# Performance work log

Hardware: AMD Instinct MI355X
Metric: run time of the kernel (lower is better)

## Reference

```python
import jax, jax.numpy as jnp
import numpy as np

EPS = 1e-6


def _mp_match(reps, att, kernel):
    """BiMPM multi-perspective match.
    reps: (B,L,D); att: (B,L,D) or (B,1,D); kernel: (M,D).
    Returns (B,L,1+M): [tanh(sum(reps*att)), tanh(sum_d reps*kernel_m*att)].
    """
    prod = reps * att                                   # (B,L,D)
    cos = jnp.tanh(jnp.sum(prod, axis=-1, keepdims=True))   # (B,L,1)
    mp = jnp.tanh(jnp.einsum('bld,md->blm', prod, kernel))  # (B,L,M)
    return jnp.concatenate([cos, mp], axis=-1)


def setup_inputs() -> dict:
    key = jax.random.key(0)
    ks = jax.random.split(key, 12)
    B, Llt, Lrt, D, M, A = 32, 128, 128, 512, 64, 128
    H = D // 2
    u = lambda k, shape: jax.random.uniform(k, shape, jnp.float32, -0.05, 0.05)  # keras 'uniform' init
    return {
        'reps_lt': jax.random.normal(ks[0], (B, Llt, D), jnp.float32),
        'h_lt_fw': jax.random.normal(ks[1], (B, H), jnp.float32),
        'h_lt_bw': jax.random.normal(ks[2], (B, H), jnp.float32),
        'reps_rt': jax.random.normal(ks[3], (B, Lrt, D), jnp.float32),
        'h_rt_fw': jax.random.normal(ks[4], (B, H), jnp.float32),
        'h_rt_bw': jax.random.normal(ks[5], (B, H), jnp.float32),
        'kernel_full': u(ks[6], (M, D)),
        'kernel_mpool': u(ks[7], (M, D)),
        'attn_w1': u(ks[8], (D, A)),
        'diag_w': u(ks[9], (A,)),
        'kernel_att': u(ks[10], (M, D)),
        'kernel_maxatt': u(ks[11], (M, D)),
    }


def reference(reps_lt, h_lt_fw, h_lt_bw, reps_rt, h_rt_fw, h_rt_bw,
              kernel_full, kernel_mpool, attn_w1, diag_w,
              kernel_att, kernel_maxatt):
    # ---- full match: each left timestep vs last BiLSTM state of right ----
    h_rt = jnp.concatenate([h_rt_fw, h_rt_bw], axis=-1)[:, None, :]  # (B,1,D)
    full = _mp_match(reps_lt, h_rt, kernel_full)                     # (B,Ll,1+M)

    # ---- max-pooling match ----
    # t[b,r,l,m] = tanh(sum_d R[b,r,d]*K[m,d]*L[b,l,d]); max over right positions r
    r_scaled = jnp.einsum('brd,md->brmd', reps_rt, kernel_mpool)     # (B,Lr,M,D)
    t = jnp.tanh(jnp.einsum('brmd,bld->brlm', r_scaled, reps_lt))    # (B,Lr,Ll,M)
    mpool = jnp.max(t, axis=1)                                       # (B,Ll,M)

    # ---- attentive match ----
    a_lt = jnp.tanh(reps_lt @ attn_w1) * diag_w                      # (B,Ll,A)
    a_rt = jnp.tanh(reps_rt @ attn_w1)                               # (B,Lr,A)
    scores = jnp.einsum('bla,bra->blr', a_lt, a_rt)                  # (B,Ll,Lr)
    probs = jax.nn.softmax(scores, axis=-1)
    att = jnp.einsum('blr,brd->bld', probs, reps_rt)                 # (B,Ll,D)
    attentive = _mp_match(reps_lt, att, kernel_att)                  # (B,Ll,1+M)

    # ---- max-attentive match ----
    num = jnp.einsum('bld,brd->blr', reps_lt, reps_rt)
    n_lt = jnp.sqrt(jnp.maximum(jnp.sum(reps_lt * reps_lt, -1), EPS))[:, :, None]
    n_rt = jnp.sqrt(jnp.maximum(jnp.sum(reps_rt * reps_rt, -1), EPS))[:, None, :]
    rel = num / n_rt / n_lt                                          # (B,Ll,Lr)
    idx = jnp.argmax(rel, axis=2)                                    # (B,Ll) int
    max_att = jnp.take_along_axis(reps_rt, idx[:, :, None], axis=1)  # (B,Ll,D)
    maxatt = _mp_match(reps_lt, max_att, kernel_maxatt)              # (B,Ll,1+M)

    return jnp.concatenate([full, mpool, attentive, maxatt], axis=-1)  # (B,Ll,3+4M)
```

## Files before the change

### kernel.cpp

```cpp
#include <hip/hip_runtime.h>
#include <hip/hip_bf16.h>
#include <math.h>
#include <stdint.h>

typedef __attribute__((ext_vector_type(8))) short short8;
typedef __attribute__((ext_vector_type(4))) float float4v;

#define DEV static __device__ __forceinline__

DEV float bflo(unsigned int u) { union { unsigned int i; float f; } v; v.i = u << 16; return v.f; }
DEV float bfhi(unsigned int u) { union { unsigned int i; float f; } v; v.i = u & 0xffff0000u; return v.f; }
DEV unsigned short f2bf(float f) {
    union { float f; unsigned int i; } v; v.f = f;
    unsigned int x = v.i;
    return (unsigned short)((x + 0x7fffu + ((x >> 16) & 1u)) >> 16);
}
DEV unsigned int pack2(float a, float b) { return (unsigned int)f2bf(a) | ((unsigned int)f2bf(b) << 16); }
#if __has_builtin(__builtin_amdgcn_cvt_pk_bf16_f32)
DEV unsigned int pack2_fast(float a, float b) {
    typedef __attribute__((ext_vector_type(2))) short short2v;
    short2v r = __builtin_amdgcn_cvt_pk_bf16_f32(a, b);
    union { short2v s; unsigned int u; } v; v.s = r; return v.u;
}
#else
DEV unsigned int pack2_fast(float a, float b) { return pack2(a, b); }
#endif
DEV void unpack8(uint4 u, float* f) {
    f[0]=bflo(u.x); f[1]=bfhi(u.x); f[2]=bflo(u.y); f[3]=bfhi(u.y);
    f[4]=bflo(u.z); f[5]=bfhi(u.z); f[6]=bflo(u.w); f[7]=bfhi(u.w);
}

DEV void async16(const unsigned short* g, unsigned short* l) {
    __builtin_amdgcn_global_load_lds(
        (const __attribute__((address_space(1))) unsigned int*)g,
        (__attribute__((address_space(3))) unsigned int*)l, 16, 0, 0);
}

__global__ __launch_bounds__(256) void prep_kernel(const float* __restrict__ lt,
                                                   const float* __restrict__ rt,
                                                   const float* __restrict__ kf,
                                                   const float* __restrict__ kmp,
                                                   const float* __restrict__ ka,
                                                   const float* __restrict__ km,
                                                   const float* __restrict__ w1,
                                                   unsigned short* __restrict__ ltb,
                                                   unsigned short* __restrict__ rtb,
                                                   unsigned short* __restrict__ kb,
                                                   unsigned short* __restrict__ w1t,
                                                   double* __restrict__ rsq) {
    __shared__ double ws2[2][2];
    __shared__ float tile[32][33];
    int bid = blockIdx.x, t = threadIdx.x;
    if (bid < 1024) {
        bool isRt = bid >= 512;
        int base = (isRt ? (bid - 512) : bid) * 8;
        int rl = t >> 7;
        int c  = t & 127;
        const float* srcb = isRt ? rt : lt;
        unsigned short* dstb = isRt ? rtb : ltb;
        #pragma unroll
        for (int p = 0; p < 4; ++p) {
            int row = base + p * 2 + rl;
            const float* src = srcb + (size_t)row * 512;
            float4 v = *(const float4*)(src + c * 4);
            ushort4 o;
            o.x = f2bf(v.x); o.y = f2bf(v.y); o.z = f2bf(v.z); o.w = f2bf(v.w);
            *(ushort4*)(dstb + (size_t)row * 512 + c * 4) = o;
            if (isRt) {
                double s = (double)v.x * v.x + (double)v.y * v.y
                         + (double)v.z * v.z + (double)v.w * v.w;
                #pragma unroll
                for (int off = 1; off < 64; off <<= 1) s += __shfl_xor(s, off, 64);
                if ((c & 63) == 0) ws2[rl][c >> 6] = s;
                __syncthreads();
                if (c == 0) rsq[row] = 1.0 / sqrt(ws2[rl][0] + ws2[rl][1]);
                __syncthreads();
            }
        }
    } else if (bid < 1152) {
        int kbk = bid - 1024;
        int ksel = kbk >> 5;
        const float* src = (ksel == 0) ? kf : (ksel == 1) ? kmp : (ksel == 2) ? ka : km;
        int off = (kbk & 31) * 1024 + t * 4;
        float4 v = *(const float4*)(src + off);
        ushort4 o;
        o.x = f2bf(v.x); o.y = f2bf(v.y); o.z = f2bf(v.z); o.w = f2bf(v.w);
        *(ushort4*)(kb + ksel * 32768 + off) = o;
    } else {
        int b2 = bid - 1152;
        int d0 = (b2 & 15) * 32, a0 = (b2 >> 4) * 32;
        int r = t >> 5, c = t & 31;
        #pragma unroll
        for (int i = 0; i < 32; i += 8)
            tile[r + i][c] = w1[(size_t)(d0 + r + i) * 128 + a0 + c];
        __syncthreads();
        #pragma unroll
        for (int i = 0; i < 32; i += 8)
            w1t[(size_t)(a0 + r + i) * 512 + d0 + c] = f2bf(tile[c][r + i]);
    }
}

__global__ __launch_bounds__(256, 3) void uber_kernel(
        const unsigned short* __restrict__ ltb,
        const unsigned short* __restrict__ rtb,
        const unsigned short* __restrict__ kmb,
        const unsigned short* __restrict__ w1t,
        const float* __restrict__ diag,
        unsigned short* __restrict__ a_all,
        const float* __restrict__ ltf,
        const float* __restrict__ rtf,
        const double* __restrict__ rsq,
        int* __restrict__ idxout,
        float* __restrict__ out) {
    __shared__ __align__(16) unsigned char smem[52224];
    int bx = blockIdx.x;
    int t = threadIdx.x;
    int wave = t >> 6, lane = t & 63;
    int q = lane >> 4, col = lane & 15, kq = q * 8;

    if (bx < 2048) {
        int xcd = bx & 7, jj = bx >> 3;
        int b = xcd * 4 + (jj >> 6);
        int m = jj & 63;
        unsigned short* ltS = (unsigned short*)smem;
        unsigned short* rtL = (unsigned short*)(smem + 16384);
        float (*mx)[2] = (float(*)[2])(smem + 16384 + 32768);
        int wl = wave & 1, wr = wave >> 1;
        const unsigned short* ltp = ltb + (size_t)b * 65536;
        const unsigned short* rtp = rtb + (size_t)b * 65536;
        const unsigned short* kr = kmb + (size_t)m * 512;
        int srow = t >> 3, cg8 = t & 7, cg = cg8 * 8;
        int gsw = (cg8 ^ (srow & 7)) * 8;
        int wbase = (t & ~63) * 8;

        #pragma unroll
        for (int it = 0; it < 4; ++it)
            async16(rtp + (size_t)(it * 32 + srow) * 512 + gsw,
                    rtL + it * 2048 + wbase);
        uint4 pk = *(const uint4*)(kr + cg);
        uint4 plt[4];
        #pragma unroll
        for (int it = 0; it < 4; ++it)
            plt[it] = *(const uint4*)(ltp + (size_t)(it * 32 + srow) * 512 + cg);

        float4v acc[4][4] = {};
        for (int k0i = 0; k0i < 8; ++k0i) {
            float kf8[8]; unpack8(pk, kf8);
            #pragma unroll
            for (int it = 0; it < 4; ++it) {
                int row = it * 32 + srow;
                float lf[8]; unpack8(plt[it], lf);
                uint4 s;
                s.x = pack2_fast(lf[0] * kf8[0], lf[1] * kf8[1]);
                s.y = pack2_fast(lf[2] * kf8[2], lf[3] * kf8[3]);
                s.z = pack2_fast(lf[4] * kf8[4], lf[5] * kf8[5]);
                s.w = pack2_fast(lf[6] * kf8[6], lf[7] * kf8[7]);
                *(uint4*)&ltS[row * 64 + gsw] = s;
            }
            __syncthreads();
            if (k0i < 7) {
                int k0n = (k0i + 1) * 64;
                int bofs = ((k0i + 1) & 1) * 8192;
                #pragma unroll
                for (int it = 0; it < 4; ++it)
                    async16(rtp + (size_t)(it * 32 + srow) * 512 + k0n + gsw,
                            rtL + bofs + it * 2048 + wbase);
                pk = *(const uint4*)(kr + k0n + cg);
                #pragma unroll
                for (int it = 0; it < 4; ++it)
                    plt[it] = *(const uint4*)(ltp + (size_t)(it * 32 + srow) * 512 + k0n + cg);
            }
            const unsigned short* rb = rtL + (k0i & 1) * 8192;
            #pragma unroll
            for (int kk = 0; kk < 64; kk += 32) {
                short8 af[4], bfr[4];
                #pragma unroll
                for (int i = 0; i < 4; ++i) {
                    int rowA = wl * 64 + i * 16 + col;
                    int slotA = ((kk >> 3) + q) ^ (rowA & 7);
                    af[i] = *(const short8*)&ltS[rowA * 64 + slotA * 8];
                }
                #pragma unroll
                for (int j = 0; j < 4; ++j) {
                    int row = wr * 64 + j * 16 + col;
                    int slot = ((kk >> 3) + q) ^ (row & 7);
                    bfr[j] = *(const short8*)&rb[row * 64 + slot * 8];
                }
                #pragma unroll
                for (int i = 0; i < 4; ++i)
                    #pragma unroll
                    for (int j = 0; j < 4; ++j)
                        acc[i][j] = __builtin_amdgcn_mfma_f32_16x16x32_bf16(af[i], bfr[j], acc[i][j], 0, 0, 0);
            }
            __syncthreads();
        }
        #pragma unroll
        for (int i = 0; i < 4; ++i)
            #pragma unroll
            for (int ii = 0; ii < 4; ++ii) {
                float v = fmaxf(fmaxf(acc[i][0][ii], acc[i][1][ii]), fmaxf(acc[i][2][ii], acc[i][3][ii]));
                #pragma unroll
                for (int off = 1; off < 16; off <<= 1) v = fmaxf(v, __shfl_xor(v, off, 64));
                if (col == 0) mx[wl * 64 + i * 16 + q * 4 + ii][wr] = v;
            }
        __syncthreads();
        if (t < 128)
            out[((size_t)(b * 128 + t)) * 259 + 65 + m] = tanhf(fmaxf(mx[t][0], mx[t][1]));

    } else if (bx < 2560) {
        int idA = bx - 2048;
        int xcd = idA & 7, jj = idA >> 3;
        int b = xcd * 4 + (jj >> 4);
        int L0 = (jj & 15) * 8;
        float* ltS = (float*)smem;
        float* buf = (float*)(smem + 16384);
        double* dvs = (double*)(smem + 49152);
        float* wv1 = (float*)(smem + 49152 + 128);
        float* wv2 = wv1 + 16;
        int* wi1 = (int*)(wv2 + 16);
        int* wi2 = wi1 + 16;
        int* candi = wi2 + 16;
        {
            int row = t >> 5, c0 = (t & 31) * 16;
            const float* src = ltf + ((size_t)(b * 128 + L0 + row)) * 512 + c0;
            #pragma unroll
            for (int i = 0; i < 4; ++i)
                *(float4*)&ltS[row * 512 + c0 + i * 4] = *(const float4*)(src + i * 4);
        }
        int lg = t >> 7;
        int rg = (t >> 2) & 31;
        int ds = t & 3;
        float acc[4][4] = {{0.f}};
        for (int p = 0; p < 8; ++p) {
            __syncthreads();
            {
                int row = t >> 1, c0 = (t & 1) * 32;
                const float* src = rtf + ((size_t)(b * 128 + row)) * 512 + p * 64 + c0;
                float f[32];
                #pragma unroll
                for (int i = 0; i < 8; ++i)
                    *(float4*)&f[i * 4] = *(const float4*)(src + i * 4);
                int base = row * 64;
                #pragma unroll
                for (int gg = 0; gg < 4; ++gg) {
                    int g = (t & 1) * 4 + gg;
                    int o = ((g ^ (row & 7)) * 8);
                    #pragma unroll
                    for (int k = 0; k < 8; ++k) buf[base + o + k] = f[gg * 8 + k];
                }
            }
            __syncthreads();
            #pragma unroll
            for (int sub = 0; sub < 2; ++sub) {
                int dloc = ds * 16 + sub * 8;
                int dglob = p * 64 + dloc;
                float a[4][8];
                #pragma unroll
                for (int i = 0; i < 4; ++i)
                    #pragma unroll
                    for (int k = 0; k < 8; ++k) a[i][k] = ltS[(lg * 4 + i) * 512 + dglob + k];
                int g = dloc >> 3;
                #pragma unroll
                for (int j = 0; j < 4; ++j) {
                    int r = rg + j * 32;
                    const float* rp = &buf[r * 64 + ((g ^ (r & 7)) * 8)];
                    float rv[8];
                    #pragma unroll
                    for (int k = 0; k < 8; ++k) rv[k] = rp[k];
                    #pragma unroll
                    for (int i = 0; i < 4; ++i)
                        #pragma unroll
                        for (int k = 0; k < 8; ++k)
                            acc[i][j] = fmaf(a[i][k], rv[k], acc[i][j]);
                }
            }
        }
        #pragma unroll
        for (int i = 0; i < 4; ++i)
            #pragma unroll
            for (int j = 0; j < 4; ++j) {
                acc[i][j] += __shfl_xor(acc[i][j], 1, 64);
                acc[i][j] += __shfl_xor(acc[i][j], 2, 64);
            }
        float v1[4], v2[4]; int i1[4], i2[4];
        #pragma unroll
        for (int i = 0; i < 4; ++i) {
            v1[i] = -3.0e38f; v2[i] = -3.0e38f; i1[i] = 0; i2[i] = 1;
            #pragma unroll
            for (int j = 0; j < 4; ++j) {
                int r = rg + j * 32;
                float s = acc[i][j] * (float)rsq[b * 128 + r];
                if (s > v1[i]) { v2[i] = v1[i]; i2[i] = i1[i]; v1[i] = s; i1[i] = r; }
                else if (s > v2[i]) { v2[i] = s; i2[i] = r; }
            }
        }
        #pragma unroll
        for (int off = 4; off < 64; off <<= 1) {
            #pragma unroll
            for (int i = 0; i < 4; ++i) {
                float u1 = __shfl_xor(v1[i], off, 64); int j1 = __shfl_xor(i1[i], off, 64);
                float u2 = __shfl_xor(v2[i], off, 64); int j2 = __shfl_xor(i2[i], off, 64);
                if (u1 > v1[i]) {
                    float ov = v1[i]; int oi = i1[i];
                    v1[i] = u1; i1[i] = j1;
                    if (u2 > ov) { v2[i] = u2; i2[i] = j2; } else { v2[i] = ov; i2[i] = oi; }
                } else if (u1 > v2[i]) { v2[i] = u1; i2[i] = j1; }
            }
        }
        if (lane == 0) {
            #pragma unroll
            for (int i = 0; i < 4; ++i) {
                int l = lg * 4 + i, h = wave & 1;
                wv1[l * 2 + h] = v1[i]; wi1[l * 2 + h] = i1[i];
                wv2[l * 2 + h] = v2[i]; wi2[l * 2 + h] = i2[i];
            }
        }
        __syncthreads();
        if (t < 8) {
            float a1 = wv1[t * 2], a2 = wv2[t * 2]; int ai1 = wi1[t * 2], ai2 = wi2[t * 2];
            float b1 = wv1[t * 2 + 1], b2 = wv2[t * 2 + 1]; int bi1 = wi1[t * 2 + 1], bi2 = wi2[t * 2 + 1];
            int ri1, ri2;
            if (b1 > a1) {
                ri1 = bi1;
                if (b2 > a1) { ri2 = bi2; } else { ri2 = ai1; }
            } else {
                ri1 = ai1;
                if (b1 > a2) { ri2 = bi1; } else { ri2 = ai2; }
            }
            candi[t * 2] = ri1; candi[t * 2 + 1] = ri2;
            (void)a2; (void)b2; (void)ai2; (void)bi2;
        }
        __syncthreads();
        {
            int dotid = t >> 4;
            int sub = t & 15;
            int l = dotid >> 1, c = dotid & 1;
            int r = candi[l * 2 + c];
            const float* lrow = ltf + ((size_t)(b * 128 + L0 + l)) * 512;
            const float* rrow = rtf + ((size_t)(b * 128 + r)) * 512;
            double s = 0.0;
            #pragma unroll 8
            for (int k = 0; k < 32; ++k) {
                int d = sub * 32 + k;
                s = fma((double)lrow[d], (double)rrow[d], s);
            }
            #pragma unroll
            for (int off = 1; off < 16; off <<= 1) s += __shfl_xor(s, off, 64);
            if (sub == 0) dvs[l * 2 + c] = s * rsq[b * 128 + r];
        }
        __syncthreads();
        if (t < 8) {
            int ia = candi[t * 2], ib = candi[t * 2 + 1];
            double va = dvs[t * 2], vb = dvs[t * 2 + 1];
            int res = (vb > va || (vb == va && ib < ia)) ? ib : ia;
            idxout[b * 128 + L0 + t] = res;
        }

    } else {
        int R0 = (bx - 2560) * 32;
        unsigned short (*aS)[72] = (unsigned short(*)[72])smem;
        unsigned short (*bS)[72] = (unsigned short(*)[72])(smem + 4608);
        float* diagS = (float*)(smem + 4608 + 18432);
        int wl = wave & 1, wr = wave >> 1;
        if (t < 128) diagS[t] = diag[t];
        const unsigned short* src = (R0 < 4096) ? (ltb + (size_t)R0 * 512) : (rtb + (size_t)(R0 - 4096) * 512);
        float4v acc[4] = {};
        for (int k0 = 0; k0 < 512; k0 += 64) {
            {
                int row = t >> 3, cg = (t & 7) * 8;
                *(uint4*)&aS[row][cg] = *(const uint4*)(src + (size_t)row * 512 + k0 + cg);
            }
            #pragma unroll
            for (int it = 0; it < 4; ++it) {
                int id = it * 256 + t;
                int row = id >> 3, cg = (id & 7) * 8;
                *(uint4*)&bS[row][cg] = *(const uint4*)(w1t + (size_t)row * 512 + k0 + cg);
            }
            __syncthreads();
            #pragma unroll
            for (int kk = 0; kk < 64; kk += 32) {
                short8 af = *(const short8*)&aS[wl * 16 + col][kk + kq];
                #pragma unroll
                for (int j = 0; j < 4; ++j) {
                    short8 bf = *(const short8*)&bS[wr * 64 + j * 16 + col][kk + kq];
                    acc[j] = __builtin_amdgcn_mfma_f32_16x16x32_bf16(af, bf, acc[j], 0, 0, 0);
                }
            }
            __syncthreads();
        }
        bool isLt = (R0 < 4096);
        #pragma unroll
        for (int j = 0; j < 4; ++j)
            #pragma unroll
            for (int ii = 0; ii < 4; ++ii) {
                int rowl = wl * 16 + q * 4 + ii;
                int n = wr * 64 + j * 16 + col;
                float v = tanhf(acc[j][ii]);
                if (isLt) v *= diagS[n];
                a_all[((size_t)(R0 + rowl)) * 128 + n] = f2bf(v);
            }
    }
}

__global__ __launch_bounds__(512, 4) void tail_kernel(
        const unsigned short* __restrict__ a_all,
        const unsigned short* __restrict__ rtb,
        const float* __restrict__ ltf,
        const unsigned short* __restrict__ kb,
        const float* __restrict__ hfw,
        const float* __restrict__ hbw,
        const int* __restrict__ idxp,
        float* __restrict__ out) {
    __shared__ __align__(16) unsigned char smem[81664];
    int bx = blockIdx.x;
    int t = threadIdx.x;
    int wave = t >> 6, lane = t & 63;
    int q = lane >> 4, col = lane & 15, kq = q * 8;

    if (bx < 256) {
        int b = bx & 31, lg = bx >> 5;
        int L0 = lg * 16;
        unsigned short (*altS)[136]  = (unsigned short(*)[136])(smem);
        unsigned short (*artS)[136]  = (unsigned short(*)[136])(smem + 4352);
        unsigned short (*rtS)[512]   = (unsigned short(*)[512])(smem + 39168);
        unsigned short (*prodsF)[520]= (unsigned short(*)[520])(smem + 55552);
        float (*P)[132]  = (float(*)[132])(smem + 72192);
        float (*pmax)[8] = (float(*)[8])(smem + 80640);
        float (*psum)[8] = (float(*)[8])(smem + 81152);
        const unsigned short* kb_att = kb + 2 * 32768;

        if (t < 256) {
            int row = t >> 4, c0 = (t & 15) * 8;
            *(uint4*)&altS[row][c0] = *(const uint4*)(a_all + ((size_t)(b * 128 + L0 + row)) * 128 + c0);
        }
        {
            int row = t >> 2, c0 = (t & 3) * 32;
            const unsigned short* src = a_all + ((size_t)(4096 + b * 128 + row)) * 128 + c0;
            #pragma unroll
            for (int i = 0; i < 4; ++i)
                *(uint4*)&artS[row][c0 + i * 8] = *(const uint4*)(src + i * 8);
        }
        __syncthreads();

        float4v acc = {};
        #pragma unroll
        for (int kk = 0; kk < 128; kk += 32) {
            short8 af = *(const short8*)&altS[col][kk + kq];
            short8 bf = *(const short8*)&artS[wave * 16 + col][kk + kq];
            acc = __builtin_amdgcn_mfma_f32_16x16x32_bf16(af, bf, acc, 0, 0, 0);
        }
        float m4[4], p4[4];
        #pragma unroll
        for (int ii = 0; ii < 4; ++ii) {
            float v = acc[ii];
            #pragma unroll
            for (int off = 1; off < 16; off <<= 1) v = fmaxf(v, __shfl_xor(v, off, 64));
            m4[ii] = v;
        }
        if (col == 0) {
            #pragma unroll
            for (int ii = 0; ii < 4; ++ii) pmax[q * 4 + ii][wave] = m4[ii];
        }
        __syncthreads();
        #pragma unroll
        for (int ii = 0; ii < 4; ++ii) {
            float M = pmax[q * 4 + ii][0];
            #pragma unroll
            for (int w = 1; w < 8; ++w) M = fmaxf(M, pmax[q * 4 + ii][w]);
            p4[ii] = expf(acc[ii] - M);
            float s = p4[ii];
            #pragma unroll
            for (int off = 1; off < 16; off <<= 1) s += __shfl_xor(s, off, 64);
            m4[ii] = s;
        }
        if (col == 0) {
            #pragma unroll
            for (int ii = 0; ii < 4; ++ii) psum[q * 4 + ii][wave] = m4[ii];
        }
        __syncthreads();
        #pragma unroll
        for (int ii = 0; ii < 4; ++ii) {
            float S = psum[q * 4 + ii][0] + psum[q * 4 + ii][1] + psum[q * 4 + ii][2] + psum[q * 4 + ii][3]
                    + psum[q * 4 + ii][4] + psum[q * 4 + ii][5] + psum[q * 4 + ii][6] + psum[q * 4 + ii][7];
            P[q * 4 + ii][wave * 16 + col] = p4[ii] / S;
        }

        int l = t >> 5, cd = t & 31;
        float a8[2][8] = {{0.f}};
        for (int rcb = 0; rcb < 128; rcb += 16) {
            __syncthreads();
            {
                int row = t >> 5, c0 = (t & 31) * 16;
                const unsigned short* src = rtb + ((size_t)(b * 128 + rcb + row)) * 512 + c0;
                *(uint4*)&rtS[row][c0] = *(const uint4*)src;
                *(uint4*)&rtS[row][c0 + 8] = *(const uint4*)(src + 8);
            }
            __syncthreads();
            for (int rr = 0; rr < 16; ++rr) {
                float pr = P[l][rcb + rr];
                #pragma unroll
                for (int pass = 0; pass < 2; ++pass) {
                    uint4 u = *(const uint4*)&rtS[rr][pass * 256 + cd * 8];
                    float f[8]; unpack8(u, f);
                    #pragma unroll
                    for (int k = 0; k < 8; ++k) a8[pass][k] += pr * f[k];
                }
            }
        }

        int grow = b * 128 + L0 + l;
        const float* ltrow = ltf + (size_t)grow * 512;
        float csum = 0.f;
        #pragma unroll
        for (int pass = 0; pass < 2; ++pass) {
            int d0 = pass * 256 + cd * 8;
            float lf[8];
            *(float4*)&lf[0] = *(const float4*)(ltrow + d0);
            *(float4*)&lf[4] = *(const float4*)(ltrow + d0 + 4);
            float pf[8];
            #pragma unroll
            for (int k = 0; k < 8; ++k) { pf[k] = lf[k] * a8[pass][k]; csum += pf[k]; }
            uint4 o;
            o.x = pack2(pf[0], pf[1]); o.y = pack2(pf[2], pf[3]);
            o.z = pack2(pf[4], pf[5]); o.w = pack2(pf[6], pf[7]);
            *(uint4*)&prodsF[l][d0] = o;
        }
        #pragma unroll
        for (int off = 1; off < 32; off <<= 1) csum += __shfl_xor(csum, off, 64);
        if (cd == 0) out[(size_t)grow * 259 + 129] = tanhf(csum);

        unsigned short* Ks = &artS[0][0];
        float* red = (float*)&rtS[0][0];
        for (int half = 0; half < 2; ++half) {
            __syncthreads();
            {
                int row = t >> 4, c0 = (t & 15) * 32;
                const unsigned short* src = kb_att + ((size_t)(half * 32 + row)) * 512 + c0;
                #pragma unroll
                for (int i = 0; i < 4; ++i)
                    *(uint4*)&Ks[row * 520 + c0 + i * 8] = *(const uint4*)(src + i * 8);
            }
            __syncthreads();
            float4v pacc[2] = {};
            #pragma unroll
            for (int kk = 0; kk < 64; kk += 32) {
                short8 af = *(const short8*)&prodsF[col][wave * 64 + kk + kq];
                #pragma unroll
                for (int j = 0; j < 2; ++j) {
                    short8 bf = *(const short8*)&Ks[(j * 16 + col) * 520 + wave * 64 + kk + kq];
                    pacc[j] = __builtin_amdgcn_mfma_f32_16x16x32_bf16(af, bf, pacc[j], 0, 0, 0);
                }
            }
            #pragma unroll
            for (int j = 0; j < 2; ++j)
                #pragma unroll
                for (int ii = 0; ii < 4; ++ii)
                    red[((wave * 2 + j) * 16 + q * 4 + ii) * 16 + col] = pacc[j][ii];
            __syncthreads();
            {
                int ll = t >> 5, jm = t & 31;
                int j = jm >> 4, mc = jm & 15;
                float s = 0.f;
                #pragma unroll
                for (int w = 0; w < 8; ++w) s += red[((w * 2 + j) * 16 + ll) * 16 + mc];
                out[((size_t)(b * 128 + L0 + ll)) * 259 + 130 + half * 32 + jm] = tanhf(s);
            }
        }

    } else {
        int idB = bx - 256;
        int lg = idB & 7, b = (idB >> 3) & 31;
        int mode = (idB >> 8) ? 2 : 0;
        int L0 = lg * 16;
        unsigned short (*prods)[520] = (unsigned short(*)[520])smem;
        unsigned short* Ks = (unsigned short*)(smem + 16640);
        float* red = (float*)(smem + 49920);
        const unsigned short* Kp = kb + (size_t)((mode == 0) ? 0 : 3 * 32768);
        int obase = (mode == 0) ? 0 : 194;

        if (t < 256) {
            int l = t >> 4, c = t & 15;
            int grow = b * 128 + L0 + l;
            const float* ltrow = ltf + (size_t)grow * 512;
            const unsigned short* avrow = 0;
            if (mode == 2) avrow = rtb + ((size_t)(b * 128 + idxp[grow])) * 512;
            float csum = 0.f;
            #pragma unroll
            for (int pass = 0; pass < 4; ++pass) {
                int d0 = pass * 128 + c * 8;
                float lf[8], af[8], pf[8];
                *(float4*)&lf[0] = *(const float4*)(ltrow + d0);
                *(float4*)&lf[4] = *(const float4*)(ltrow + d0 + 4);
                if (mode == 0) {
                    const float* h = (d0 < 256) ? (hfw + b * 256 + d0) : (hbw + b * 256 + d0 - 256);
                    *(float4*)&af[0] = *(const float4*)h;
                    *(float4*)&af[4] = *(const float4*)(h + 4);
                } else {
                    uint4 av = *(const uint4*)(avrow + d0);
                    unpack8(av, af);
                }
                #pragma unroll
                for (int k = 0; k < 8; ++k) { pf[k] = lf[k] * af[k]; csum += pf[k]; }
                uint4 o;
                o.x = pack2(pf[0], pf[1]); o.y = pack2(pf[2], pf[3]);
                o.z = pack2(pf[4], pf[5]); o.w = pack2(pf[6], pf[7]);
                *(uint4*)&prods[l][d0] = o;
            }
            #pragma unroll
            for (int off = 1; off < 16; off <<= 1) csum += __shfl_xor(csum, off, 64);
            if (c == 0) out[(size_t)grow * 259 + obase] = tanhf(csum);
        }
        for (int half = 0; half < 2; ++half) {
            {
                int row = t >> 4, c0 = (t & 15) * 32;
                const unsigned short* src = Kp + ((size_t)(half * 32 + row)) * 512 + c0;
                #pragma unroll
                for (int i = 0; i < 4; ++i)
                    *(uint4*)&Ks[row * 520 + c0 + i * 8] = *(const uint4*)(src + i * 8);
            }
            __syncthreads();
            float4v acc2[2] = {};
            #pragma unroll
            for (int kk = 0; kk < 64; kk += 32) {
                short8 af = *(const short8*)&prods[col][wave * 64 + kk + kq];
                #pragma unroll
                for (int j = 0; j < 2; ++j) {
                    short8 bf = *(const short8*)&Ks[(j * 16 + col) * 520 + wave * 64 + kk + kq];
                    acc2[j] = __builtin_amdgcn_mfma_f32_16x16x32_bf16(af, bf, acc2[j], 0, 0, 0);
                }
            }
            #pragma unroll
            for (int j = 0; j < 2; ++j)
                #pragma unroll
                for (int ii = 0; ii < 4; ++ii)
                    red[((wave * 2 + j) * 16 + q * 4 + ii) * 16 + col] = acc2[j][ii];
            __syncthreads();
            {
                int ll = t >> 5, jm = t & 31;
                int j = jm >> 4, mc = jm & 15;
                float s = 0.f;
                #pragma unroll
                for (int w = 0; w < 8; ++w) s += red[((w * 2 + j) * 16 + ll) * 16 + mc];
                out[((size_t)(b * 128 + L0 + ll)) * 259 + obase + 1 + half * 32 + jm] = tanhf(s);
            }
            __syncthreads();
        }
    }
}

extern "C" void kernel_launch(void* const* d_in, const int* in_sizes, int n_in,
                              void* d_out, int out_size, void* d_ws, size_t ws_size,
                              hipStream_t stream) {
    const float* lt  = (const float*)d_in[0];
    const float* rt  = (const float*)d_in[3];
    const float* hfw = (const float*)d_in[4];
    const float* hbw = (const float*)d_in[5];
    const float* kf  = (const float*)d_in[6];
    const float* kmp = (const float*)d_in[7];
    const float* w1  = (const float*)d_in[8];
    const float* dia = (const float*)d_in[9];
    const float* ka  = (const float*)d_in[10];
    const float* km  = (const float*)d_in[11];
    float* out = (float*)d_out;

    char* wsb = (char*)d_ws;
    unsigned short* ltb16 = (unsigned short*)(wsb);
    unsigned short* rtb16 = (unsigned short*)(wsb + 4194304);
    unsigned short* kb16  = (unsigned short*)(wsb + 8388608);
    unsigned short* w1t   = (unsigned short*)(wsb + 8650752);
    unsigned short* a_all = (unsigned short*)(wsb + 8781824);
    double*         rsq   = (double*)(wsb + 15073280);
    int*            idx   = (int*)(wsb + 15106048);

    prep_kernel<<<1216, 256, 0, stream>>>(lt, rt, kf, kmp, ka, km, w1, ltb16, rtb16, kb16, w1t, rsq);
    uber_kernel<<<2816, 256, 0, stream>>>(ltb16, rtb16, kb16 + 32768, w1t, dia, a_all,
                                          lt, rt, rsq, idx, out);
    tail_kernel<<<768, 512, 0, stream>>>(a_all, rtb16, lt, kb16, hfw, hbw, idx, out);
}
```

Measured before the change: 188.1 us.

## Compute attentive weighted sum with bf16 MFMA using transposed right reps

Replaces the scalar FMA loop that builds the attention-weighted right representation in the tail kernel with bf16 MFMA tiles. Probabilities are stored as bf16 in shared memory. The prep kernel gains a transpose of reps_rt into a d-major bf16 buffer that is loaded asynchronously with an XOR swizzle. This trades an extra prep pass and bf16 rounding of probabilities for much less ALU work in the tail.

```diff
diff --git a/kernel.cpp b/kernel.cpp
--- a/kernel.cpp
+++ b/kernel.cpp
@@ -47,6 +47,7 @@
                                                    unsigned short* __restrict__ rtb,
                                                    unsigned short* __restrict__ kb,
                                                    unsigned short* __restrict__ w1t,
+                                                   unsigned short* __restrict__ rtbT,
                                                    double* __restrict__ rsq) {
     __shared__ double ws2[2][2];
     __shared__ float tile[32][33];
@@ -86,7 +87,7 @@
         ushort4 o;
         o.x = f2bf(v.x); o.y = f2bf(v.y); o.z = f2bf(v.z); o.w = f2bf(v.w);
         *(ushort4*)(kb + ksel * 32768 + off) = o;
-    } else {
+    } else if (bid < 1216) {
         int b2 = bid - 1152;
         int d0 = (b2 & 15) * 32, a0 = (b2 >> 4) * 32;
         int r = t >> 5, c = t & 31;
@@ -97,6 +98,20 @@
         #pragma unroll
         for (int i = 0; i < 32; i += 8)
             w1t[(size_t)(a0 + r + i) * 512 + d0 + c] = f2bf(tile[c][r + i]);
+    } else {
+        int b3 = bid - 1216;
+        int b = b3 >> 6;
+        int tid = b3 & 63;
+        int d0 = (tid & 15) * 32;
+        int r0 = (tid >> 4) * 32;
+        int r = t >> 5, c = t & 31;
+        #pragma unroll
+        for (int i = 0; i < 32; i += 8)
+            tile[r + i][c] = rt[(size_t)(b * 128 + r0 + r + i) * 512 + d0 + c];
+        __syncthreads();
+        #pragma unroll
+        for (int i = 0; i < 32; i += 8)
+            rtbT[(size_t)(b * 512 + d0 + r + i) * 128 + r0 + c] = f2bf(tile[c][r + i]);
     }
 }
 
@@ -405,6 +420,7 @@
 __global__ __launch_bounds__(512, 4) void tail_kernel(
         const unsigned short* __restrict__ a_all,
         const unsigned short* __restrict__ rtb,
+        const unsigned short* __restrict__ rtbT,
         const float* __restrict__ ltf,
         const unsigned short* __restrict__ kb,
         const float* __restrict__ hfw,
@@ -422,9 +438,7 @@
         int L0 = lg * 16;
         unsigned short (*altS)[136]  = (unsigned short(*)[136])(smem);
         unsigned short (*artS)[136]  = (unsigned short(*)[136])(smem + 4352);
-        unsigned short (*rtS)[512]   = (unsigned short(*)[512])(smem + 39168);
         unsigned short (*prodsF)[520]= (unsigned short(*)[520])(smem + 55552);
-        float (*P)[132]  = (float(*)[132])(smem + 72192);
         float (*pmax)[8] = (float(*)[8])(smem + 80640);
         float (*psum)[8] = (float(*)[8])(smem + 81152);
         const unsigned short* kb_att = kb + 2 * 32768;
@@ -478,35 +492,47 @@
             for (int ii = 0; ii < 4; ++ii) psum[q * 4 + ii][wave] = m4[ii];
         }
         __syncthreads();
+        unsigned short* Pb = (unsigned short*)smem;
         #pragma unroll
         for (int ii = 0; ii < 4; ++ii) {
             float S = psum[q * 4 + ii][0] + psum[q * 4 + ii][1] + psum[q * 4 + ii][2] + psum[q * 4 + ii][3]
                     + psum[q * 4 + ii][4] + psum[q * 4 + ii][5] + psum[q * 4 + ii][6] + psum[q * 4 + ii][7];
-            P[q * 4 + ii][wave * 16 + col] = p4[ii] / S;
+            Pb[(q * 4 + ii) * 136 + wave * 16 + col] = f2bf(p4[ii] / S);
+        }
+
+        unsigned short* Bc = (unsigned short*)(smem + 4352);
+        float* attF = (float*)(smem + 39168);
+        const unsigned short* rtT = rtbT + (size_t)b * 65536;
+        for (int cc = 0; cc < 4; ++cc) {
+            #pragma unroll
+            for (int i = 0; i < 4; ++i) {
+                int rid = i * 32 + (t >> 4);
+                int d   = (rid >> 4) * 64 + cc * 16 + (rid & 15);
+                int sg  = (t & 15) ^ (rid & 15);
+                async16(rtT + (size_t)d * 128 + sg * 8, Bc + i * 4096 + t * 8);
+            }
+            __syncthreads();
+            float4v pacc = {};
+            #pragma unroll
+            for (int ks = 0; ks < 4; ++ks) {
+                short8 afP = *(const short8*)&Pb[col * 136 + ks * 32 + kq];
+                short8 bfB = *(const short8*)&Bc[(wave * 16 + col) * 128 + (((ks * 4 + q) ^ col) * 8)];
+                pacc = __builtin_amdgcn_mfma_f32_16x16x32_bf16(afP, bfB, pacc, 0, 0, 0);
+            }
+            #pragma unroll
+            for (int ii = 0; ii < 4; ++ii)
+                attF[(q * 4 + ii) * 512 + wave * 64 + cc * 16 + col] = pacc[ii];
+            __syncthreads();
         }
 
         int l = t >> 5, cd = t & 31;
-        float a8[2][8] = {{0.f}};
-        for (int rcb = 0; rcb < 128; rcb += 16) {
-            __syncthreads();
-            {
-                int row = t >> 5, c0 = (t & 31) * 16;
-                const unsigned short* src = rtb + ((size_t)(b * 128 + rcb + row)) * 512 + c0;
-                *(uint4*)&rtS[row][c0] = *(const uint4*)src;
-                *(uint4*)&rtS[row][c0 + 8] = *(const uint4*)(src + 8);
-            }
-            __syncthreads();
-            for (int rr = 0; rr < 16; ++rr) {
-                float pr = P[l][rcb + rr];
-                #pragma unroll
-                for (int pass = 0; pass < 2; ++pass) {
-                    uint4 u = *(const uint4*)&rtS[rr][pass * 256 + cd * 8];
-                    float f[8]; unpack8(u, f);
-                    #pragma unroll
-                    for (int k = 0; k < 8; ++k) a8[pass][k] += pr * f[k];
-                }
-            }
-        }
+        float a8[2][8];
+        #pragma unroll
+        for (int pass = 0; pass < 2; ++pass) {
+            *(float4*)&a8[pass][0] = *(const float4*)&attF[l * 512 + pass * 256 + cd * 8];
+            *(float4*)&a8[pass][4] = *(const float4*)&attF[l * 512 + pass * 256 + cd * 8 + 4];
+        }
+        __syncthreads();
 
         int grow = b * 128 + L0 + l;
         const float* ltrow = ltf + (size_t)grow * 512;
@@ -530,7 +556,7 @@
         if (cd == 0) out[(size_t)grow * 259 + 129] = tanhf(csum);
 
         unsigned short* Ks = &artS[0][0];
-        float* red = (float*)&rtS[0][0];
+        float* red = (float*)(smem + 39168);
         for (int half = 0; half < 2; ++half) {
             __syncthreads();
             {
@@ -669,11 +695,12 @@
     unsigned short* kb16  = (unsigned short*)(wsb + 8388608);
     unsigned short* w1t   = (unsigned short*)(wsb + 8650752);
     unsigned short* a_all = (unsigned short*)(wsb + 8781824);
+    unsigned short* rtbT  = (unsigned short*)(wsb + 10878976);
     double*         rsq   = (double*)(wsb + 15073280);
     int*            idx   = (int*)(wsb + 15106048);
 
-    prep_kernel<<<1216, 256, 0, stream>>>(lt, rt, kf, kmp, ka, km, w1, ltb16, rtb16, kb16, w1t, rsq);
+    prep_kernel<<<3264, 256, 0, stream>>>(lt, rt, kf, kmp, ka, km, w1, ltb16, rtb16, kb16, w1t, rtbT, rsq);
     uber_kernel<<<2816, 256, 0, stream>>>(ltb16, rtb16, kb16 + 32768, w1t, dia, a_all,
                                           lt, rt, rsq, idx, out);
-    tail_kernel<<<768, 512, 0, stream>>>(a_all, rtb16, lt, kb16, hfw, hbw, idx, out);
+    tail_kernel<<<768, 512, 0, stream>>>(a_all, rtb16, rtbT, lt, kb16, hfw, hbw, idx, out);
 }
```

Result: faster. 174.4 us (-7.3%).
